# Optimization experiments

Hardware: AMD Instinct MI355X
Metric: run time of the kernel (lower is better)

## Reference

```python
import jax, jax.numpy as jnp
import numpy as np

B, S, D, H = 2, 2048, 1024, 16
HD = D // H  # head_dim = 64
NEG = -1.0e9


def setup_inputs() -> dict:
    key = jax.random.key(0)
    ks = jax.random.split(key, 9)
    s = 1.0 / np.sqrt(D)
    return {
        "x": jax.random.normal(ks[0], (B, S, D), jnp.float32),
        "mask": jnp.ones((B, S), jnp.float32),
        "Wq": jax.random.normal(ks[1], (D, D), jnp.float32) * s,
        "bq": jnp.zeros((D,), jnp.float32),
        "Wk": jax.random.normal(ks[2], (D, D), jnp.float32) * s,
        "bk": jnp.zeros((D,), jnp.float32),
        "Wv": jax.random.normal(ks[3], (D, D), jnp.float32) * s,
        "bv": jnp.zeros((D,), jnp.float32),
        "Wo": jax.random.normal(ks[4], (D, D), jnp.float32) * s,
        "bo": jnp.zeros((D,), jnp.float32),
    }


def reference(x, mask, Wq, bq, Wk, bk, Wv, bv, Wo, bo):
    # QKV projections -> [B, H, S, HD]
    def proj(t, W, b):
        return (t @ W + b).reshape(B, S, H, HD).transpose(0, 2, 1, 3)

    q = proj(x, Wq, bq)
    k = proj(x, Wk, bk)
    v = proj(x, Wv, bv)

    scores = jnp.einsum("bhqd,bhkd->bhqk", q, k) / jnp.sqrt(jnp.asarray(HD, x.dtype))
    # causal mask: scores * m + (1-m) * -1e9 (matches original exactly)
    cm = jnp.tril(jnp.ones((S, S), x.dtype))[None, None]
    scores = scores * cm + (1.0 - cm) * NEG
    # 2D padding mask branch
    scores = scores + (1.0 - mask[:, None, None, :]) * NEG

    attn = jax.nn.softmax(scores, axis=-1)
    out = jnp.einsum("bhqk,bhkd->bqhd", attn, v).reshape(B, S, D)
    return out @ Wo + bo
```

## Files before the change

### kernel.cpp

```cpp
#include <hip/hip_runtime.h>
#include <hip/hip_bf16.h>
#include <cstdint>
#include <cstddef>

typedef __attribute__((ext_vector_type(8))) short short8;
typedef __attribute__((ext_vector_type(4))) float floatx4;
typedef __attribute__((ext_vector_type(2))) unsigned int uintx2;

#define MFMA16(a, b, c) __builtin_amdgcn_mfma_f32_16x16x32_bf16((a), (b), (c), 0, 0, 0)
#define LOG2E 1.44269504088896340736f
#define EXP2(x) __builtin_amdgcn_exp2f(x)

__device__ __forceinline__ unsigned short f2bf(float f) {
  unsigned int u = __builtin_bit_cast(unsigned int, f);
  u += 0x7fffu + ((u >> 16) & 1u);
  return (unsigned short)(u >> 16);
}

__device__ __forceinline__ unsigned int pk2(float a, float b) {
  float2 f; f.x = a; f.y = b;
  __hip_bfloat162 h = __float22bfloat162_rn(f);
  unsigned int u;
  __builtin_memcpy(&u, &h, 4);
  return u;
}

typedef __attribute__((address_space(1))) void gvoid_t;
typedef __attribute__((address_space(3))) void svoid_t;
__device__ __forceinline__ void gload_lds16(const void* g, void* l) {
  __builtin_amdgcn_global_load_lds((gvoid_t*)(uintptr_t)g, (svoid_t*)(uintptr_t)l, 16, 0, 0);
}

__global__ void convert_x(const float* __restrict__ x, unsigned short* __restrict__ xb) {
  int i = (blockIdx.x * 256 + threadIdx.x) * 4;
  floatx4 v = *(const floatx4*)(x + i);
  uintx2 o;
  o[0] = pk2(v[0], v[1]);
  o[1] = pk2(v[2], v[3]);
  *(uintx2*)(xb + i) = o;
}

__global__ void transpose_w(const float* __restrict__ Wq, const float* __restrict__ Wk,
                            const float* __restrict__ Wv, const float* __restrict__ Wo,
                            unsigned short* __restrict__ Wqkvt, unsigned short* __restrict__ Wot) {
  __shared__ float tile[32][33];
  int z = blockIdx.z;
  const float* W = (z == 0) ? Wq : (z == 1) ? Wk : (z == 2) ? Wv : Wo;
  unsigned short* out = (z == 3) ? Wot : (Wqkvt + (size_t)z * 1024 * 1024);
  int n0 = blockIdx.x * 32, k0 = blockIdx.y * 32;
  int tx = threadIdx.x, ty = threadIdx.y;
#pragma unroll
  for (int j = 0; j < 4; ++j)
    tile[ty + j * 8][tx] = W[(size_t)(k0 + ty + j * 8) * 1024 + n0 + tx];
  __syncthreads();
#pragma unroll
  for (int j = 0; j < 4; ++j)
    out[(size_t)(n0 + ty + j * 8) * 1024 + k0 + tx] = f2bf(tile[tx][ty + j * 8]);
}

#define GEMM_PROLOGUE()                                                        \
  __shared__ __align__(16) unsigned short As[128 * 64];                        \
  __shared__ __align__(16) unsigned short Bs[128 * 64];                        \
  const int tid = threadIdx.x;                                                 \
  const int lane = tid & 63;                                                   \
  const int wid = tid >> 6;                                                    \
  const int col = lane & 15;                                                   \
  const int quad = lane >> 4;                                                  \
  const int m0 = blockIdx.x * 128;                                             \
  const int n0 = blockIdx.y * 128;                                             \
  const int wm = wid >> 1;                                                     \
  const int wn = wid & 1;                                                      \
  floatx4 acc[4][4];                                                           \
  _Pragma("unroll") for (int i = 0; i < 4; ++i)                                \
      _Pragma("unroll") for (int j = 0; j < 4; ++j)                            \
          acc[i][j] = (floatx4)(0.f);                                          \
  _Pragma("unroll 1") for (int kt = 0; kt < 16; ++kt) {                        \
    __syncthreads();                                                           \
    _Pragma("unroll") for (int call = 0; call < 4; ++call) {                   \
      int c = call * 256 + tid;                                                \
      int r = c >> 3, ch = c & 7;                                              \
      gload_lds16(A + (size_t)(m0 + r) * 1024 + kt * 64 + ((ch ^ (r & 7)) * 8),\
                  As + (size_t)(call * 256 + wid * 64) * 8);                   \
      gload_lds16(Bt + (size_t)(n0 + r) * 1024 + kt * 64 + ((ch ^ (r & 7)) * 8),\
                  Bs + (size_t)(call * 256 + wid * 64) * 8);                   \
    }                                                                          \
    __syncthreads();                                                           \
    _Pragma("unroll") for (int ks = 0; ks < 2; ++ks) {                         \
      short8 af[4], bf[4];                                                     \
      _Pragma("unroll") for (int rt = 0; rt < 4; ++rt) {                       \
        int row = wm * 64 + rt * 16 + col;                                     \
        af[rt] = *(const short8*)&As[row * 64 + (((ks * 4 + quad) ^ (row & 7)) * 8)]; \
      }                                                                        \
      _Pragma("unroll") for (int ct = 0; ct < 4; ++ct) {                       \
        int row = wn * 64 + ct * 16 + col;                                     \
        bf[ct] = *(const short8*)&Bs[row * 64 + (((ks * 4 + quad) ^ (row & 7)) * 8)]; \
      }                                                                        \
      _Pragma("unroll") for (int rt = 0; rt < 4; ++rt)                         \
          _Pragma("unroll") for (int ct = 0; ct < 4; ++ct)                     \
              acc[rt][ct] = MFMA16(af[rt], bf[ct], acc[rt][ct]);               \
    }                                                                          \
  }

__global__ __launch_bounds__(256, 3)
void gemm_qkv(const unsigned short* __restrict__ A, const unsigned short* __restrict__ Bt,
              const float* __restrict__ bq, const float* __restrict__ bk,
              const float* __restrict__ bv,
              unsigned short* __restrict__ Qo, unsigned short* __restrict__ Ko,
              unsigned short* __restrict__ Vo) {
  GEMM_PROLOGUE()
  const int nseg = n0 >> 10;
  const float* bias = (nseg == 0) ? bq : ((nseg == 1) ? bk : bv);
#pragma unroll
  for (int rt = 0; rt < 4; ++rt) {
#pragma unroll
    for (int ct = 0; ct < 4; ++ct) {
      int mg = m0 + wm * 64 + rt * 16 + quad * 4;
      int ng = n0 + wn * 64 + ct * 16 + col;
      int c = ng & 1023;
      int hh = c >> 6, hd = c & 63;
      int b_ = mg >> 11, s = mg & 2047;
      float bb = bias[c];
      if (nseg == 2) {
        uintx2 pk;
        pk[0] = pk2(acc[rt][ct][0] + bb, acc[rt][ct][1] + bb);
        pk[1] = pk2(acc[rt][ct][2] + bb, acc[rt][ct][3] + bb);
        *(uintx2*)&Vo[(size_t)(b_ * 16 + hh) * 131072 + (size_t)hd * 2048 + s] = pk;
      } else {
        unsigned short* dst =
            ((nseg == 0) ? Qo : Ko) + ((size_t)(b_ * 16 + hh) * 2048 + s) * 64 + hd;
        float scl = (nseg == 0) ? (0.125f * LOG2E) : 1.0f;
#pragma unroll
        for (int i = 0; i < 4; ++i) dst[(size_t)i * 64] = f2bf((acc[rt][ct][i] + bb) * scl);
      }
    }
  }
}

__global__ __launch_bounds__(256, 3)
void gemm_out(const unsigned short* __restrict__ A, const unsigned short* __restrict__ Bt,
              const float* __restrict__ bo, float* __restrict__ Out) {
  GEMM_PROLOGUE()
#pragma unroll
  for (int rt = 0; rt < 4; ++rt) {
#pragma unroll
    for (int ct = 0; ct < 4; ++ct) {
      int mg = m0 + wm * 64 + rt * 16 + quad * 4;
      int ng = n0 + wn * 64 + ct * 16 + col;
      float bb = bo[ng];
#pragma unroll
      for (int i = 0; i < 4; ++i)
        Out[(size_t)(mg + i) * 1024 + ng] = acc[rt][ct][i] + bb;
    }
  }
}

__global__ __launch_bounds__(256, 3)
void flash_attn(const unsigned short* __restrict__ Q, const unsigned short* __restrict__ K,
                const unsigned short* __restrict__ Vt, const float* __restrict__ mask,
                unsigned short* __restrict__ O) {
  __shared__ __align__(16) unsigned short Ks[128 * 64];
  __shared__ __align__(16) unsigned short Vs[64 * 128];
  __shared__ __align__(16) unsigned short Ps[64 * 128];
  __shared__ int mflag[16];

  const int tid = threadIdx.x;
  const int lane = tid & 63;
  const int wid = tid >> 6;
  const int col = lane & 15;
  const int quad = lane >> 4;
  const int j = 31 - (int)(blockIdx.x >> 5);
  const int bh = blockIdx.x & 31;
  const int b = bh >> 4, h = bh & 15;
  const int q0 = j * 64;
  const int tdiag = j >> 1;

  const unsigned short* Qp = Q + (size_t)bh * 2048 * 64;
  const unsigned short* Kp = K + (size_t)bh * 2048 * 64;
  const unsigned short* Vp = Vt + (size_t)bh * 64 * 2048;
  const float* mp = mask + b * 2048;

  const int lr8 = lane >> 3, lc8 = lane & 7;
  const floatx4 fzero = (floatx4)(0.f);
  const floatx4 fone = (floatx4)(1.f);

  const int kr = tid >> 1, kh = (tid & 1) * 4;
  const int vr = tid >> 2, vh = (tid & 3) * 4;
  const unsigned short* Kg = Kp + (size_t)kr * 64 + kh * 8;
  const unsigned short* Vg = Vp + (size_t)vr * 2048 + vh * 8;
  unsigned short* Kl = Ks + kr * 64;
  unsigned short* Vl = Vs + vr * 128;

#pragma unroll
  for (int i = 0; i < 2; ++i) {
    int seg = wid * 2 + i;
    int r = seg * 8 + lr8;
    gload_lds16(Qp + (size_t)(q0 + r) * 64 + ((lc8 ^ (r & 7)) * 8), Ps + seg * 512);
  }
  if (tid < 16) mflag[tid] = 0;
  short8 kreg[4], vreg[4];
#pragma unroll
  for (int c = 0; c < 4; ++c) kreg[c] = *(const short8*)(Kg + c * 8);
#pragma unroll
  for (int c = 0; c < 4; ++c) vreg[c] = *(const short8*)(Vg + c * 8);
  __syncthreads();
  short8 qf[2];
  {
    int q = wid * 16 + col;
#pragma unroll
    for (int ks = 0; ks < 2; ++ks)
      qf[ks] = *(const short8*)&Ps[q * 64 + (((ks * 4 + quad) ^ (q & 7)) * 8)];
  }
  for (int c = tid; c < (tdiag + 1) * 32; c += 256) {
    floatx4 mm = *(const floatx4*)&mp[c * 4];
    if (mm[0] != 1.f || mm[1] != 1.f || mm[2] != 1.f || mm[3] != 1.f)
      atomicOr(&mflag[c >> 5], 1);
  }
  __syncthreads();

  floatx4 o[4];
#pragma unroll
  for (int dt = 0; dt < 4; ++dt) o[dt] = fzero;
  float mrow = -1e30f;
  float lrow = 0.f;

#pragma unroll 1
  for (int t = 0; t <= tdiag; ++t) {
    if (t > 0) __syncthreads();
#pragma unroll
    for (int c = 0; c < 4; ++c) *(short8*)(Kl + (((kh + c) ^ (kr & 7)) * 8)) = kreg[c];
#pragma unroll
    for (int c = 0; c < 4; ++c) *(short8*)(Vl + (((vh + c) ^ (vr & 15)) * 8)) = vreg[c];
    if (t < tdiag) {
#pragma unroll
      for (int c = 0; c < 4; ++c)
        kreg[c] = *(const short8*)(Kg + (size_t)(t + 1) * 8192 + c * 8);
#pragma unroll
      for (int c = 0; c < 4; ++c)
        vreg[c] = *(const short8*)(Vg + (t + 1) * 128 + c * 8);
    }
    __syncthreads();

    floatx4 sc[8];
#pragma unroll
    for (int rt = 0; rt < 8; ++rt) {
      int krr = rt * 16 + col;
      short8 kf0 = *(const short8*)&Ks[krr * 64 + ((quad ^ (col & 7)) * 8)];
      short8 kf1 = *(const short8*)&Ks[krr * 64 + (((4 + quad) ^ (col & 7)) * 8)];
      floatx4 s0 = MFMA16(kf0, qf[0], fzero);
      sc[rt] = MFMA16(kf1, qf[1], s0);
    }
    if (__builtin_amdgcn_readfirstlane(mflag[t])) {
#pragma unroll
      for (int rt = 0; rt < 8; ++rt) {
        floatx4 mm = *(const floatx4*)&mp[t * 128 + rt * 16 + quad * 4];
        sc[rt] += (fone - mm) * (-1.0e9f * LOG2E);
      }
    }
    if (t == tdiag) {
      int qg = q0 + wid * 16 + col;
#pragma unroll
      for (int rt = 0; rt < 8; ++rt)
#pragma unroll
        for (int i = 0; i < 4; ++i)
          if (t * 128 + rt * 16 + quad * 4 + i > qg) sc[rt][i] = -1.0e9f * LOG2E;
    }

    float mt = -1e30f;
#pragma unroll
    for (int rt = 0; rt < 8; ++rt)
      mt = fmaxf(mt, fmaxf(fmaxf(sc[rt][0], sc[rt][1]), fmaxf(sc[rt][2], sc[rt][3])));
    mt = fmaxf(mt, __shfl_xor(mt, 16));
    mt = fmaxf(mt, __shfl_xor(mt, 32));

    const bool skip = (__all(mt - mrow <= 8.0f) != 0);
    float mn = mrow;
    if (!skip) {
      mn = fmaxf(mrow, mt);
      float alpha = EXP2(mrow - mn);
      mrow = mn;
      lrow *= alpha;
#pragma unroll
      for (int dt = 0; dt < 4; ++dt) o[dt] *= alpha;
    }
    float sum = 0.f;
#pragma unroll
    for (int rt = 0; rt < 8; ++rt)
#pragma unroll
      for (int i = 0; i < 4; ++i) {
        float p = EXP2(sc[rt][i] - mn);
        sc[rt][i] = p;
        sum += p;
      }
    sum += __shfl_xor(sum, 16);
    sum += __shfl_xor(sum, 32);
    lrow += sum;
    {
      int qloc = wid * 16 + col;
#pragma unroll
      for (int rt = 0; rt < 8; ++rt) {
        uintx2 w;
        w[0] = pk2(sc[rt][0], sc[rt][1]);
        w[1] = pk2(sc[rt][2], sc[rt][3]);
        int chunk = (rt * 2 + (quad >> 1)) ^ col;
        *(uintx2*)&Ps[qloc * 128 + chunk * 8 + (quad & 1) * 4] = w;
      }
    }
#pragma unroll
    for (int ks = 0; ks < 4; ++ks) {
      int ch = ks * 4 + quad;
      short8 pf = *(const short8*)&Ps[(wid * 16 + col) * 128 + ((ch ^ col) * 8)];
#pragma unroll
      for (int dt = 0; dt < 4; ++dt) {
        short8 vf = *(const short8*)&Vs[(dt * 16 + col) * 128 + ((ch ^ col) * 8)];
        o[dt] = MFMA16(vf, pf, o[dt]);
      }
    }
  }

  {
    float inv = 1.0f / lrow;
    int qg = q0 + wid * 16 + col;
    unsigned short* dst = O + ((size_t)(b * 2048 + qg)) * 1024 + h * 64;
#pragma unroll
    for (int dt = 0; dt < 4; ++dt) {
      uintx2 pk;
      pk[0] = pk2(o[dt][0] * inv, o[dt][1] * inv);
      pk[1] = pk2(o[dt][2] * inv, o[dt][3] * inv);
      *(uintx2*)&dst[dt * 16 + quad * 4] = pk;
    }
  }
}

extern "C" void kernel_launch(void* const* d_in, const int* in_sizes, int n_in,
                              void* d_out, int out_size, void* d_ws, size_t ws_size,
                              hipStream_t stream) {
  (void)in_sizes; (void)n_in; (void)out_size; (void)ws_size;
  const float* x  = (const float*)d_in[0];
  const float* mask = (const float*)d_in[1];
  const float* Wq = (const float*)d_in[2];
  const float* bq = (const float*)d_in[3];
  const float* Wk = (const float*)d_in[4];
  const float* bk = (const float*)d_in[5];
  const float* Wv = (const float*)d_in[6];
  const float* bv = (const float*)d_in[7];
  const float* Wo = (const float*)d_in[8];
  const float* bo = (const float*)d_in[9];
  float* out = (float*)d_out;

  char* ws = (char*)d_ws;
  unsigned short* xb    = (unsigned short*)(ws);
  unsigned short* Wqkvt = (unsigned short*)(ws + (8u << 20));
  unsigned short* Wot   = (unsigned short*)(ws + (14u << 20));
  unsigned short* Qb    = (unsigned short*)(ws + (16u << 20));
  unsigned short* Kb    = (unsigned short*)(ws + (24u << 20));
  unsigned short* Vtb   = (unsigned short*)(ws + (32u << 20));
  unsigned short* Ao    = (unsigned short*)(ws + (40u << 20));

  convert_x<<<4096, 256, 0, stream>>>(x, xb);
  transpose_w<<<dim3(32, 32, 4), dim3(32, 8), 0, stream>>>(Wq, Wk, Wv, Wo, Wqkvt, Wot);
  gemm_qkv<<<dim3(32, 24), 256, 0, stream>>>(xb, Wqkvt, bq, bk, bv, Qb, Kb, Vtb);
  flash_attn<<<dim3(1024), 256, 0, stream>>>(Qb, Kb, Vtb, mask, Ao);
  gemm_out<<<dim3(32, 8), 256, 0, stream>>>(Ao, Wot, bo, out);
}
```

Baseline: 186.1 us.

## Reuse K buffer for P, load K/V via direct-to-LDS, rebalance causal block order

The separate P shared buffer is removed; P is written into the K tile after an added barrier, cutting LDS use so occupancy can rise from 3 to 4 blocks per CU. K/V tiles are now fetched with global-to-LDS loads each iteration instead of being prefetched into registers, which drops register pressure but also removes the overlap of loads with compute. The mask flag check now uses a per-wave ballot into a bitmask instead of shared atomics. Block ordering interleaves long and short causal rows across four slots for load balance, and MFMA sections get raised wave priority.

```diff
diff --git a/kernel.cpp b/kernel.cpp
--- a/kernel.cpp
+++ b/kernel.cpp
@@ -154,22 +154,23 @@
   }
 }
 
-__global__ __launch_bounds__(256, 3)
+__global__ __launch_bounds__(256, 4)
 void flash_attn(const unsigned short* __restrict__ Q, const unsigned short* __restrict__ K,
                 const unsigned short* __restrict__ Vt, const float* __restrict__ mask,
                 unsigned short* __restrict__ O) {
   __shared__ __align__(16) unsigned short Ks[128 * 64];
   __shared__ __align__(16) unsigned short Vs[64 * 128];
-  __shared__ __align__(16) unsigned short Ps[64 * 128];
-  __shared__ int mflag[16];
 
   const int tid = threadIdx.x;
   const int lane = tid & 63;
   const int wid = tid >> 6;
   const int col = lane & 15;
   const int quad = lane >> 4;
-  const int j = 31 - (int)(blockIdx.x >> 5);
-  const int bh = blockIdx.x & 31;
+  const int slot = (int)(blockIdx.x >> 8);
+  const int g = (int)(blockIdx.x & 255);
+  const int h8 = g >> 5;
+  const int bh = g & 31;
+  const int j = (slot == 0) ? (31 - h8) : (slot == 1) ? h8 : (slot == 2) ? (23 - h8) : (8 + h8);
   const int b = bh >> 4, h = bh & 15;
   const int q0 = j * 64;
   const int tdiag = j >> 1;
@@ -180,42 +181,30 @@
   const float* mp = mask + b * 2048;
 
   const int lr8 = lane >> 3, lc8 = lane & 7;
+  const int lr16 = lane >> 4, lc16 = lane & 15;
   const floatx4 fzero = (floatx4)(0.f);
   const floatx4 fone = (floatx4)(1.f);
-
-  const int kr = tid >> 1, kh = (tid & 1) * 4;
-  const int vr = tid >> 2, vh = (tid & 3) * 4;
-  const unsigned short* Kg = Kp + (size_t)kr * 64 + kh * 8;
-  const unsigned short* Vg = Vp + (size_t)vr * 2048 + vh * 8;
-  unsigned short* Kl = Ks + kr * 64;
-  unsigned short* Vl = Vs + vr * 128;
 
 #pragma unroll
   for (int i = 0; i < 2; ++i) {
     int seg = wid * 2 + i;
     int r = seg * 8 + lr8;
-    gload_lds16(Qp + (size_t)(q0 + r) * 64 + ((lc8 ^ (r & 7)) * 8), Ps + seg * 512);
-  }
-  if (tid < 16) mflag[tid] = 0;
-  short8 kreg[4], vreg[4];
-#pragma unroll
-  for (int c = 0; c < 4; ++c) kreg[c] = *(const short8*)(Kg + c * 8);
-#pragma unroll
-  for (int c = 0; c < 4; ++c) vreg[c] = *(const short8*)(Vg + c * 8);
+    gload_lds16(Qp + (size_t)(q0 + r) * 64 + ((lc8 ^ (r & 7)) * 8), Ks + seg * 512);
+  }
   __syncthreads();
   short8 qf[2];
   {
     int q = wid * 16 + col;
 #pragma unroll
     for (int ks = 0; ks < 2; ++ks)
-      qf[ks] = *(const short8*)&Ps[q * 64 + (((ks * 4 + quad) ^ (q & 7)) * 8)];
-  }
-  for (int c = tid; c < (tdiag + 1) * 32; c += 256) {
-    floatx4 mm = *(const floatx4*)&mp[c * 4];
-    if (mm[0] != 1.f || mm[1] != 1.f || mm[2] != 1.f || mm[3] != 1.f)
-      atomicOr(&mflag[c >> 5], 1);
-  }
-  __syncthreads();
+      qf[ks] = *(const short8*)&Ks[q * 64 + (((ks * 4 + quad) ^ (q & 7)) * 8)];
+  }
+  unsigned int mbits = 0;
+  for (int t = 0; t <= tdiag; ++t) {
+    float2 mv = *(const float2*)&mp[t * 128 + lane * 2];
+    unsigned long long bb = __ballot(mv.x != 1.f || mv.y != 1.f);
+    mbits |= (bb ? 1u : 0u) << t;
+  }
 
   floatx4 o[4];
 #pragma unroll
@@ -225,31 +214,35 @@
 
 #pragma unroll 1
   for (int t = 0; t <= tdiag; ++t) {
-    if (t > 0) __syncthreads();
-#pragma unroll
-    for (int c = 0; c < 4; ++c) *(short8*)(Kl + (((kh + c) ^ (kr & 7)) * 8)) = kreg[c];
-#pragma unroll
-    for (int c = 0; c < 4; ++c) *(short8*)(Vl + (((vh + c) ^ (vr & 15)) * 8)) = vreg[c];
-    if (t < tdiag) {
-#pragma unroll
-      for (int c = 0; c < 4; ++c)
-        kreg[c] = *(const short8*)(Kg + (size_t)(t + 1) * 8192 + c * 8);
-#pragma unroll
-      for (int c = 0; c < 4; ++c)
-        vreg[c] = *(const short8*)(Vg + (t + 1) * 128 + c * 8);
-    }
     __syncthreads();
+#pragma unroll
+    for (int i = 0; i < 4; ++i) {
+      int seg = wid * 4 + i;
+      int r = seg * 8 + lr8;
+      gload_lds16(Kp + (size_t)(t * 128 + r) * 64 + ((lc8 ^ (r & 7)) * 8), Ks + seg * 512);
+    }
+#pragma unroll
+    for (int i = 0; i < 4; ++i) {
+      int seg = wid * 4 + i;
+      int r = seg * 4 + lr16;
+      gload_lds16(Vp + (size_t)r * 2048 + t * 128 + ((lc16 ^ (r & 15)) * 8), Vs + seg * 512);
+    }
+    __syncthreads();
 
     floatx4 sc[8];
+    __builtin_amdgcn_s_setprio(1);
 #pragma unroll
     for (int rt = 0; rt < 8; ++rt) {
-      int krr = rt * 16 + col;
-      short8 kf0 = *(const short8*)&Ks[krr * 64 + ((quad ^ (col & 7)) * 8)];
-      short8 kf1 = *(const short8*)&Ks[krr * 64 + (((4 + quad) ^ (col & 7)) * 8)];
+      int kr = rt * 16 + col;
+      short8 kf0 = *(const short8*)&Ks[kr * 64 + ((quad ^ (col & 7)) * 8)];
+      short8 kf1 = *(const short8*)&Ks[kr * 64 + (((4 + quad) ^ (col & 7)) * 8)];
       floatx4 s0 = MFMA16(kf0, qf[0], fzero);
       sc[rt] = MFMA16(kf1, qf[1], s0);
     }
-    if (__builtin_amdgcn_readfirstlane(mflag[t])) {
+    __builtin_amdgcn_s_setprio(0);
+    __syncthreads();
+
+    if (__builtin_amdgcn_readfirstlane(mbits >> t) & 1) {
 #pragma unroll
       for (int rt = 0; rt < 8; ++rt) {
         floatx4 mm = *(const floatx4*)&mp[t * 128 + rt * 16 + quad * 4];
@@ -294,6 +287,7 @@
     sum += __shfl_xor(sum, 16);
     sum += __shfl_xor(sum, 32);
     lrow += sum;
+
     {
       int qloc = wid * 16 + col;
 #pragma unroll
@@ -302,19 +296,21 @@
         w[0] = pk2(sc[rt][0], sc[rt][1]);
         w[1] = pk2(sc[rt][2], sc[rt][3]);
         int chunk = (rt * 2 + (quad >> 1)) ^ col;
-        *(uintx2*)&Ps[qloc * 128 + chunk * 8 + (quad & 1) * 4] = w;
-      }
-    }
+        *(uintx2*)&Ks[qloc * 128 + chunk * 8 + (quad & 1) * 4] = w;
+      }
+    }
+    __builtin_amdgcn_s_setprio(1);
 #pragma unroll
     for (int ks = 0; ks < 4; ++ks) {
       int ch = ks * 4 + quad;
-      short8 pf = *(const short8*)&Ps[(wid * 16 + col) * 128 + ((ch ^ col) * 8)];
+      short8 pf = *(const short8*)&Ks[(wid * 16 + col) * 128 + ((ch ^ col) * 8)];
 #pragma unroll
       for (int dt = 0; dt < 4; ++dt) {
         short8 vf = *(const short8*)&Vs[(dt * 16 + col) * 128 + ((ch ^ col) * 8)];
         o[dt] = MFMA16(vf, pf, o[dt]);
       }
     }
+    __builtin_amdgcn_s_setprio(0);
   }
 
   {
```

Result: no change. 183.6 us (-1.3%).
